# Kernel tuning notes

Measured on AMD Instinct MI355X. Metric: run time of the kernel, lower is better.

Reference implementation:

```python
import jax, jax.numpy as jnp
import numpy as np

GRID = 28
P = GRID * GRID  # 784 grid points
BY = 1.0 / 13.5  # grid spacing from DTMWeightWrapperLayer(by=1/13.5)
_c = BY * np.stack(np.meshgrid(np.arange(GRID), np.arange(GRID), indexing='ij'), -1).reshape(P, 2).astype(np.float32)
_D2np = ((_c[:, None, :] - _c[None, :, :]) ** 2).sum(-1)
_ORDERnp = np.argsort(_D2np, axis=1)  # per-grid-point neighbor order (constant)
D2S = jnp.asarray(np.take_along_axis(_D2np, _ORDERnp, axis=1), dtype=jnp.float32)  # [P,P] sorted sq dists
ORDER = jnp.asarray(_ORDERnp, dtype=jnp.int32)
TSEQ_A = jnp.asarray(np.linspace(0.06, 0.3, 25), dtype=jnp.float32); KK_A = (0, 1)
TSEQ_B = jnp.asarray(np.linspace(0.14, 0.4, 27), dtype=jnp.float32); KK_B = (0, 1, 2)

def _conv(x, k):
    return jax.lax.conv_general_dilated(x, k, (1, 1), 'SAME', dimension_numbers=('NHWC', 'HWIO', 'NHWC'))

def _dtm(w, m0):
    # distance-to-measure: w [B,P] nonneg weights on the 28x28 grid -> dtm values [B,P]
    ws = w[:, ORDER]                      # [B,P,P] weights ordered by distance from each grid point
    cum = jnp.cumsum(ws, axis=-1)
    m0W = m0 * jnp.sum(w, axis=-1)[:, None, None]  # mass threshold per sample
    eff = jnp.clip(m0W - (cum - ws), 0.0, ws)      # effective weight used from each neighbor
    return jnp.sqrt(jnp.sum(eff * D2S[None], axis=-1) / m0W[:, :, 0])

def _topo(f, tseq, kk, W, b):
    # persistence-landscape features: lambda_k(t) = k-th largest tent value over grid points
    tmax = tseq[-1]
    tent = jnp.maximum(0.0, jnp.minimum(tseq[None, :, None] - f[:, None, :], (tmax - tseq)[None, :, None]))  # [B,T,P]
    top, _ = jax.lax.top_k(tent, max(kk) + 1)       # [B,T,kmax]
    lam = top[..., jnp.asarray(kk)]                 # [B,T,|KK|]
    return lam.reshape(f.shape[0], -1) @ W + b

def setup_inputs() -> dict:
    key = jax.random.key(0)
    ks = jax.random.split(key, 16)
    r = lambda i, s: (0.05 * jax.random.normal(ks[i], s)).astype(jnp.float32)
    z = lambda n: jnp.zeros((n,), jnp.float32)
    return {
        'x': jax.random.uniform(ks[0], (16, 28, 28, 1), jnp.float32),
        'k11': r(1, (3, 3, 1, 32)), 'cb11': z(32), 'k12': r(2, (3, 3, 32, 1)), 'cb12': z(1),
        'k31': r(3, (3, 3, 1, 32)), 'cb31': z(32), 'k32': r(4, (3, 3, 32, 1)), 'cb32': z(1),
        'k41': r(5, (3, 3, 1, 32)), 'cb41': z(32), 'k42': r(6, (3, 3, 32, 1)), 'cb42': z(1),
        'W33': r(7, (50, 16)), 'b33': z(16), 'W43': r(8, (81, 16)), 'b43': z(16),
        'W5': r(9, (50, 16)), 'b5': z(16), 'W6': r(10, (81, 16)), 'b6': z(16),
        'W7': r(11, (848, 64)), 'b7': z(64), 'W8': r(12, (64, 10)), 'b8': z(10),
    }

def reference(x, k11, cb11, k12, cb12, k31, cb31, k32, cb32, k41, cb41, k42, cb42,
              W33, b33, W43, b43, W5, b5, W6, b6, W7, b7, W8, b8):
    relu = jax.nn.relu
    B = 16
    # CNN branch on raw image
    x1 = relu(_conv(relu(_conv(x, k11) + cb11), k12) + cb12).reshape(B, P)
    # DTM functions on the grid
    x2 = x.reshape(B, P)
    x2_1 = _dtm(x2, 0.05)
    x2_2 = _dtm(x2, 0.2)
    # CNN on DTM(m0=0.05) then topo layer
    x3 = relu(_conv(relu(_conv(x2_1.reshape(B, GRID, GRID, 1), k31) + cb31), k32) + cb32).reshape(B, P)
    x3 = relu(_topo(x3, TSEQ_A, KK_A, W33, b33))
    # CNN on DTM(m0=0.2) then topo layer
    x4 = relu(_conv(relu(_conv(x2_2.reshape(B, GRID, GRID, 1), k41) + cb41), k42) + cb42).reshape(B, P)
    x4 = relu(_topo(x4, TSEQ_B, KK_B, W43, b43))
    # topo layers directly on DTM functions
    x5 = relu(_topo(x2_1, TSEQ_A, KK_A, W5, b5))
    x6 = relu(_topo(x2_2, TSEQ_B, KK_B, W6, b6))
    xc = jnp.concatenate((x1, x3, x4, x5, x6), axis=-1)  # [16,848]
    return relu(xc @ W7 + b7) @ W8 + b8  # [16,10]
```

## Files before the change

### kernel.cpp

```cpp
#include <hip/hip_runtime.h>
#include <math.h>

#define GRID 28
#define NP 784

struct PairTab { unsigned int pk[NP]; float d2[NP]; };
constexpr PairTab make_pairs() {
    PairTab t{};
    int cnt[1459] = {};
    for (int di = 0; di < GRID; ++di)
        for (int dj = 0; dj < GRID; ++dj) cnt[di*di + dj*dj]++;
    int off[1459] = {};
    int acc = 0;
    for (int s = 0; s < 1459; ++s) { off[s] = acc; acc += cnt[s]; }
    const double BY2 = (1.0/13.5) * (1.0/13.5);
    for (int di = 0; di < GRID; ++di)
        for (int dj = 0; dj < GRID; ++dj) {
            int s = di*di + dj*dj;
            int o = off[s]++;
            t.pk[o] = (unsigned)((di << 8) | dj);
            t.d2[o] = (float)((double)s * BY2);
        }
    return t;
}
__constant__ PairTab d_PT = make_pairs();

__device__ void conv_band(const float* __restrict__ in,
                          const float* __restrict__ kA, const float* __restrict__ cbA,
                          const float* __restrict__ kB, const float* __restrict__ cbB,
                          float* __restrict__ outImg, int r0, float* smem)
{
    float* inl = smem;
    float* kAl = inl + 224;
    float* kBl = kAl + 288;
    float* cbl = kBl + 288;
    float* h   = cbl + 32;
    const int tid = threadIdx.x;
    const float cbB0 = cbB[0];

    if (tid < 288) { kAl[tid] = kA[tid]; kBl[tid] = kB[tid]; }
    else if (tid < 320) cbl[tid - 288] = cbA[tid - 288];
    else if (tid < 320 + 8*GRID) {
        const int i = tid - 320;
        const int lr = i / GRID, xx = i % GRID;
        const int y = r0 - 2 + lr;
        inl[i] = ((unsigned)y < GRID) ? in[y*GRID + xx] : 0.f;
    }
    __syncthreads();

    for (int o = tid; o < 6*GRID*32; o += 1024) {
        const int c = o & 31;
        const int pos = o >> 5;
        const int xx = pos % GRID;
        const int lr = pos / GRID;
        const int y = r0 - 1 + lr;
        if ((unsigned)y < GRID) {
            float a = cbl[c];
            #pragma unroll
            for (int dy = 0; dy < 3; ++dy) {
                const int iy = y + dy - 1;
                if ((unsigned)iy >= GRID) continue;
                const int il = iy - (r0 - 2);
                #pragma unroll
                for (int dx = 0; dx < 3; ++dx) {
                    const int ix = xx + dx - 1;
                    if ((unsigned)ix < GRID)
                        a = fmaf(inl[il*GRID + ix], kAl[(dy*3 + dx)*32 + c], a);
                }
            }
            h[(lr*GRID + xx)*33 + c] = fmaxf(a, 0.f);
        }
    }
    __syncthreads();

    if (tid < 4*4*GRID) {
        const int o = tid >> 2, part = tid & 3;
        const int xx = o % GRID, ly = o / GRID;
        const int y = r0 + ly;
        float a = 0.f;
        #pragma unroll
        for (int dy = 0; dy < 3; ++dy) {
            const int yy = y + dy - 1;
            if ((unsigned)yy >= GRID) continue;
            const int lr = yy - (r0 - 1);
            #pragma unroll
            for (int dx = 0; dx < 3; ++dx) {
                const int x2 = xx + dx - 1;
                if ((unsigned)x2 >= GRID) continue;
                const float* hb = &h[(lr*GRID + x2)*33 + part*8];
                const float* kb = &kBl[(dy*3 + dx)*32 + part*8];
                #pragma unroll
                for (int c = 0; c < 8; ++c) a += hb[c] * kb[c];
            }
        }
        a += __shfl_xor(a, 1, 64);
        a += __shfl_xor(a, 2, 64);
        if (part == 0) outImg[y*GRID + xx] = fmaxf(a + cbB0, 0.f);
    }
}

__global__ __launch_bounds__(1024) void k1_kernel(const float* __restrict__ x,
        const float* __restrict__ k11, const float* __restrict__ cb11,
        const float* __restrict__ k12, const float* __restrict__ cb12,
        float* __restrict__ ws)
{
    __shared__ float smem[6376];
    const int blk = blockIdx.x;
    const int tid = threadIdx.x;

    if (blk < 112) {
        const int img = blk / 7, band = blk % 7;
        conv_band(x + img*NP, k11, cb11, k12, cb12, ws + 25088 + img*NP, band*4, smem);
        return;
    }

    float* wimg = smem;
    float* red  = smem + 784;
    float* out1 = ws;
    float* out2 = ws + 12544;
    const int dblk = blk - 112;
    const int img = dblk / 49, grp = dblk % 49;
    const int w = tid >> 6, lane = tid & 63;

    float v = 0.f;
    if (tid < NP) { v = x[img*NP + tid]; wimg[tid] = v; }
    for (int off = 32; off; off >>= 1) v += __shfl_down(v, off, 64);
    if (lane == 0) red[w] = v;
    __syncthreads();
    float sumw = 0.f;
    #pragma unroll
    for (int i = 0; i < 16; ++i) sumw += red[i];

    const int pix = grp*16 + w;
    const int pr = pix / GRID, pc = pix % GRID;
    const float m0W1 = 0.05f * sumw;
    const float m0W2 = 0.2f  * sumw;
    float a1 = 0.f, a2 = 0.f, carry = 0.f;

    for (int k0 = 0; k0 < NP; k0 += 64) {
        const int idx = k0 + lane;
        const int ii  = idx < NP ? idx : NP-1;
        const unsigned p = d_PT.pk[ii];
        const float dd   = d_PT.d2[ii];
        const int di = (int)(p >> 8);
        const int dj = (int)(p & 255u);
        const int dG = di * GRID;
        const bool rpOK = (pr + di) < GRID;
        const bool rmOK = pr >= di;
        const bool cpOK = (pc + dj) < GRID;
        const bool cmOK = pc >= dj;
        float Wg = 0.f;
        if (rpOK && cpOK)               Wg += wimg[pix + dG + dj];
        if (dj && rpOK && cmOK)         Wg += wimg[pix + dG - dj];
        if (di && rmOK && cpOK)         Wg += wimg[pix - dG + dj];
        if (di && dj && rmOK && cmOK)   Wg += wimg[pix - dG - dj];
        if (idx >= NP) Wg = 0.f;
        float incl = Wg;
        #pragma unroll
        for (int d = 1; d < 64; d <<= 1) {
            const float t = __shfl_up(incl, d, 64);
            if (lane >= d) incl += t;
        }
        const float cumb = carry + (incl - Wg);
        const float e1 = fminf(fmaxf(m0W1 - cumb, 0.f), Wg);
        const float e2 = fminf(fmaxf(m0W2 - cumb, 0.f), Wg);
        a1 = fmaf(e1, dd, a1);
        a2 = fmaf(e2, dd, a2);
        carry += __shfl(incl, 63, 64);
        if (carry >= m0W2) break;
    }
    for (int m = 32; m; m >>= 1) { a1 += __shfl_xor(a1, m, 64); a2 += __shfl_xor(a2, m, 64); }
    if (lane == 0) {
        out1[img*NP + pix] = sqrtf(a1 / m0W1);
        out2[img*NP + pix] = sqrtf(a2 / m0W2);
    }
}

__global__ __launch_bounds__(1024) void k2_kernel(
        const float* __restrict__ k31, const float* __restrict__ cb31,
        const float* __restrict__ k32, const float* __restrict__ cb32,
        const float* __restrict__ k41, const float* __restrict__ cb41,
        const float* __restrict__ k42, const float* __restrict__ cb42,
        float* __restrict__ ws)
{
    __shared__ float smem[6376];
    const int blk = blockIdx.x;
    const float* x2_1 = ws;
    const float* x2_2 = ws + 12544;
    float* x3c = ws + 37632;
    float* x4c = ws + 50176;

    if (blk < 112) {
        const int img = blk / 7, band = blk % 7;
        conv_band(x2_1 + img*NP, k31, cb31, k32, cb32, x3c + img*NP, band*4, smem);
    } else {
        const int c = blk - 112;
        const int img = c / 7, band = c % 7;
        conv_band(x2_2 + img*NP, k41, cb41, k42, cb42, x4c + img*NP, band*4, smem);
    }
}

__device__ __forceinline__ float tseqA(int i) {
    if (i == 24) return 0.3f;
    return (float)((double)i * ((0.3 - 0.06)/24.0) + 0.06);
}
__device__ __forceinline__ float tseqB(int i) {
    if (i == 26) return 0.4f;
    return (float)((double)i * ((0.4 - 0.14)/26.0) + 0.14);
}

__device__ __forceinline__ void merge3(float& m0, float& m1, float& m2,
                                       float b0, float b1, float b2) {
    float r0, r1, r2;
    if (m0 <= b0) {
        r0 = m0;
        if (m1 <= b0) { r1 = m1; r2 = fminf(m2, b0); }
        else          { r1 = b0; r2 = fminf(m1, b1); }
    } else {
        r0 = b0;
        if (b1 <= m0) { r1 = b1; r2 = fminf(b2, m0); }
        else          { r1 = m0; r2 = fminf(m1, b1); }
    }
    m0 = r0; m1 = r1; m2 = r2;
}

__global__ __launch_bounds__(1024) void tail_kernel(
        const float* __restrict__ W33, const float* __restrict__ b33,
        const float* __restrict__ W43, const float* __restrict__ b43,
        const float* __restrict__ W5,  const float* __restrict__ b5,
        const float* __restrict__ W6,  const float* __restrict__ b6,
        const float* __restrict__ W7,  const float* __restrict__ b7,
        const float* __restrict__ W8,  const float* __restrict__ b8,
        const float* __restrict__ ws,  float* __restrict__ out)
{
    __shared__ float xc[848];
    __shared__ float part[1024];
    __shared__ float h7[64];
    __shared__ float fsh[16];
    const int b = blockIdx.x, tid = threadIdx.x;
    const int w = tid >> 6, lane = tid & 63;
    const float* x2_1 = ws;
    const float* x2_2 = ws + 12544;
    const float* x1o  = ws + 25088;
    const float* x3c  = ws + 37632;
    const float* x4c  = ws + 50176;

    if (tid < NP) xc[tid] = x1o[b*NP + tid];

    if (w < 4) {
        const float* src = (w == 0) ? x3c : (w == 1) ? x4c : (w == 2) ? x2_1 : x2_2;
        src += b*NP;
        float m0 = INFINITY, m1 = INFINITY, m2 = INFINITY;
        for (int i = lane; i < NP; i += 64) {
            const float v = src[i];
            if (v < m0)      { m2 = m1; m1 = m0; m0 = v; }
            else if (v < m1) { m2 = m1; m1 = v; }
            else if (v < m2) { m2 = v; }
        }
        for (int mask = 1; mask <= 32; mask <<= 1) {
            const float b0 = __shfl_xor(m0, mask, 64);
            const float b1 = __shfl_xor(m1, mask, 64);
            const float b2 = __shfl_xor(m2, mask, 64);
            merge3(m0, m1, m2, b0, b1, b2);
        }
        if (lane == 0) { fsh[w*3+0] = m0; fsh[w*3+1] = m1; fsh[w*3+2] = m2; }
    }
    __syncthreads();

    if (w < 4) {
        const int g = lane >> 4, j = lane & 15;
        const float f0 = fsh[w*3+0], f1 = fsh[w*3+1], f2 = fsh[w*3+2];
        float acc = 0.f;
        if (w == 0 || w == 2) {
            const float* Wm = (w == 0) ? W33 : W5;
            for (int i = g; i < 50; i += 4) {
                const int t = i >> 1, k = i & 1;
                const float ts = tseqA(t);
                const float fk = k ? f1 : f0;
                const float lam = fmaxf(fminf(ts - fk, 0.3f - ts), 0.f);
                acc = fmaf(lam, Wm[i*16 + j], acc);
            }
        } else {
            const float* Wm = (w == 1) ? W43 : W6;
            for (int i = g; i < 81; i += 4) {
                const int t = i / 3, k = i - t*3;
                const float ts = tseqB(t);
                const float fk = (k == 0) ? f0 : (k == 1 ? f1 : f2);
                const float lam = fmaxf(fminf(ts - fk, 0.4f - ts), 0.f);
                acc = fmaf(lam, Wm[i*16 + j], acc);
            }
        }
        acc += __shfl_xor(acc, 16, 64);
        acc += __shfl_xor(acc, 32, 64);
        if (lane < 16) {
            const float* bv = (w == 0) ? b33 : (w == 1) ? b43 : (w == 2) ? b5 : b6;
            xc[784 + w*16 + lane] = fmaxf(acc + bv[lane], 0.f);
        }
    }
    __syncthreads();

    {
        float acc = 0.f;
        const int i0 = w * 53;
        for (int i = i0; i < i0 + 53; ++i) acc = fmaf(xc[i], W7[i*64 + lane], acc);
        part[w*64 + lane] = acc;
    }
    __syncthreads();
    if (tid < 64) {
        float s = b7[tid];
        #pragma unroll
        for (int k = 0; k < 16; ++k) s += part[k*64 + tid];
        h7[tid] = fmaxf(s, 0.f);
    }
    __syncthreads();

    if (w < 10) {
        float a2 = h7[lane] * W8[lane*10 + w];
        for (int m = 32; m; m >>= 1) a2 += __shfl_down(a2, m, 64);
        if (lane == 0) out[b*10 + w] = a2 + b8[w];
    }
}

extern "C" void kernel_launch(void* const* d_in, const int* in_sizes, int n_in,
                              void* d_out, int out_size, void* d_ws, size_t ws_size,
                              hipStream_t stream)
{
    const float* x    = (const float*)d_in[0];
    const float* k11  = (const float*)d_in[1];
    const float* cb11 = (const float*)d_in[2];
    const float* k12  = (const float*)d_in[3];
    const float* cb12 = (const float*)d_in[4];
    const float* k31  = (const float*)d_in[5];
    const float* cb31 = (const float*)d_in[6];
    const float* k32  = (const float*)d_in[7];
    const float* cb32 = (const float*)d_in[8];
    const float* k41  = (const float*)d_in[9];
    const float* cb41 = (const float*)d_in[10];
    const float* k42  = (const float*)d_in[11];
    const float* cb42 = (const float*)d_in[12];
    const float* W33  = (const float*)d_in[13];
    const float* b33  = (const float*)d_in[14];
    const float* W43  = (const float*)d_in[15];
    const float* b43  = (const float*)d_in[16];
    const float* W5   = (const float*)d_in[17];
    const float* b5   = (const float*)d_in[18];
    const float* W6   = (const float*)d_in[19];
    const float* b6   = (const float*)d_in[20];
    const float* W7   = (const float*)d_in[21];
    const float* b7   = (const float*)d_in[22];
    const float* W8   = (const float*)d_in[23];
    const float* b8   = (const float*)d_in[24];
    float* ws  = (float*)d_ws;
    float* out = (float*)d_out;

    k1_kernel  <<<dim3(896), dim3(1024), 0, stream>>>(x, k11, cb11, k12, cb12, ws);
    k2_kernel  <<<dim3(224), dim3(1024), 0, stream>>>(k31, cb31, k32, cb32,
                                                      k41, cb41, k42, cb42, ws);
    tail_kernel<<<dim3(16),  dim3(1024), 0, stream>>>(W33, b33, W43, b43, W5, b5, W6, b6,
                                                      W7, b7, W8, b8, ws, out);
}
```

Baseline: 32.62 us.

## Rework conv band with padded tiles, register sliding window and float4 loads

The conv band now keeps its input and hidden tiles zero-padded, so the boundary checks in the inner loops go away. Each thread holds the nine first-layer weights and a 3x3 input window in registers and slides the window down six rows, instead of reloading everything from shared memory for each output. The second layer reads the padded hidden tile, which has a stride of 36, with float4 loads, and the launch bounds add a min-blocks hint. The cost is more shared memory and a zero-fill pass over the hidden buffer.

New measurement: 31.36 us. 3.9% less time.

```diff
diff --git a/kernel.cpp b/kernel.cpp
--- a/kernel.cpp
+++ b/kernel.cpp
@@ -25,72 +25,75 @@
 }
 __constant__ PairTab d_PT = make_pairs();
 
+#define CB_SMEM 7328
 __device__ void conv_band(const float* __restrict__ in,
                           const float* __restrict__ kA, const float* __restrict__ cbA,
                           const float* __restrict__ kB, const float* __restrict__ cbB,
                           float* __restrict__ outImg, int r0, float* smem)
 {
     float* inl = smem;
-    float* kAl = inl + 224;
+    float* kAl = inl + 240;
     float* kBl = kAl + 288;
     float* cbl = kBl + 288;
     float* h   = cbl + 32;
     const int tid = threadIdx.x;
     const float cbB0 = cbB[0];
 
-    if (tid < 288) { kAl[tid] = kA[tid]; kBl[tid] = kB[tid]; }
+    if (tid < 288)      { kAl[tid] = kA[tid]; kBl[tid] = kB[tid]; }
     else if (tid < 320) cbl[tid - 288] = cbA[tid - 288];
-    else if (tid < 320 + 8*GRID) {
+    else if (tid < 560) {
         const int i = tid - 320;
-        const int lr = i / GRID, xx = i % GRID;
-        const int y = r0 - 2 + lr;
-        inl[i] = ((unsigned)y < GRID) ? in[y*GRID + xx] : 0.f;
-    }
-    __syncthreads();
-
-    for (int o = tid; o < 6*GRID*32; o += 1024) {
-        const int c = o & 31;
-        const int pos = o >> 5;
-        const int xx = pos % GRID;
-        const int lr = pos / GRID;
-        const int y = r0 - 1 + lr;
-        if ((unsigned)y < GRID) {
-            float a = cbl[c];
-            #pragma unroll
-            for (int dy = 0; dy < 3; ++dy) {
-                const int iy = y + dy - 1;
-                if ((unsigned)iy >= GRID) continue;
-                const int il = iy - (r0 - 2);
-                #pragma unroll
-                for (int dx = 0; dx < 3; ++dx) {
-                    const int ix = xx + dx - 1;
-                    if ((unsigned)ix < GRID)
-                        a = fmaf(inl[il*GRID + ix], kAl[(dy*3 + dx)*32 + c], a);
-                }
+        const int lr = i / 30, col = i % 30;
+        const int y = r0 - 2 + lr, ix = col - 1;
+        inl[i] = ((unsigned)y < GRID && (unsigned)ix < GRID) ? in[y*GRID + ix] : 0.f;
+    }
+    {
+        float4* h4 = (float4*)h;
+        for (int i = tid; i < 6480/4; i += 1024) h4[i] = make_float4(0.f,0.f,0.f,0.f);
+    }
+    __syncthreads();
+
+    if (tid < 896) {
+        const int c = tid & 31, xx = tid >> 5;
+        float ka0 = kAl[0*32+c], ka1 = kAl[1*32+c], ka2 = kAl[2*32+c];
+        float ka3 = kAl[3*32+c], ka4 = kAl[4*32+c], ka5 = kAl[5*32+c];
+        float ka6 = kAl[6*32+c], ka7 = kAl[7*32+c], ka8 = kAl[8*32+c];
+        const float bias = cbl[c];
+        float w00 = inl[0*30+xx], w01 = inl[0*30+xx+1], w02 = inl[0*30+xx+2];
+        float w10 = inl[1*30+xx], w11 = inl[1*30+xx+1], w12 = inl[1*30+xx+2];
+        float w20 = inl[2*30+xx], w21 = inl[2*30+xx+1], w22 = inl[2*30+xx+2];
+        #pragma unroll
+        for (int s = 0; s < 6; ++s) {
+            const int y = r0 - 1 + s;
+            float a = bias;
+            a = fmaf(w00, ka0, a); a = fmaf(w01, ka1, a); a = fmaf(w02, ka2, a);
+            a = fmaf(w10, ka3, a); a = fmaf(w11, ka4, a); a = fmaf(w12, ka5, a);
+            a = fmaf(w20, ka6, a); a = fmaf(w21, ka7, a); a = fmaf(w22, ka8, a);
+            if ((unsigned)y < GRID) h[(s*30 + xx + 1)*36 + c] = fmaxf(a, 0.f);
+            if (s < 5) {
+                w00 = w10; w01 = w11; w02 = w12;
+                w10 = w20; w11 = w21; w12 = w22;
+                w20 = inl[(s+3)*30+xx]; w21 = inl[(s+3)*30+xx+1]; w22 = inl[(s+3)*30+xx+2];
             }
-            h[(lr*GRID + xx)*33 + c] = fmaxf(a, 0.f);
-        }
-    }
-    __syncthreads();
-
-    if (tid < 4*4*GRID) {
-        const int o = tid >> 2, part = tid & 3;
-        const int xx = o % GRID, ly = o / GRID;
+        }
+    }
+    __syncthreads();
+
+    if (tid < 448) {
+        const int part = tid & 3, o = tid >> 2;
+        const int xx = o % 28, ly = o / 28;
         const int y = r0 + ly;
         float a = 0.f;
         #pragma unroll
         for (int dy = 0; dy < 3; ++dy) {
-            const int yy = y + dy - 1;
-            if ((unsigned)yy >= GRID) continue;
-            const int lr = yy - (r0 - 1);
             #pragma unroll
             for (int dx = 0; dx < 3; ++dx) {
-                const int x2 = xx + dx - 1;
-                if ((unsigned)x2 >= GRID) continue;
-                const float* hb = &h[(lr*GRID + x2)*33 + part*8];
-                const float* kb = &kBl[(dy*3 + dx)*32 + part*8];
-                #pragma unroll
-                for (int c = 0; c < 8; ++c) a += hb[c] * kb[c];
+                const float4* hb = (const float4*)&h[((ly+dy)*30 + xx+dx)*36 + part*8];
+                const float4* kb = (const float4*)&kBl[(dy*3+dx)*32 + part*8];
+                const float4 h0 = hb[0], h1 = hb[1];
+                const float4 k0 = kb[0], k1 = kb[1];
+                a += h0.x*k0.x; a += h0.y*k0.y; a += h0.z*k0.z; a += h0.w*k0.w;
+                a += h1.x*k1.x; a += h1.y*k1.y; a += h1.z*k1.z; a += h1.w*k1.w;
             }
         }
         a += __shfl_xor(a, 1, 64);
@@ -99,12 +102,12 @@
     }
 }
 
-__global__ __launch_bounds__(1024) void k1_kernel(const float* __restrict__ x,
+__global__ __launch_bounds__(1024, 8) void k1_kernel(const float* __restrict__ x,
         const float* __restrict__ k11, const float* __restrict__ cb11,
         const float* __restrict__ k12, const float* __restrict__ cb12,
         float* __restrict__ ws)
 {
-    __shared__ float smem[6376];
+    __shared__ float smem[CB_SMEM];
     const int blk = blockIdx.x;
     const int tid = threadIdx.x;
 
@@ -176,14 +179,14 @@
     }
 }
 
-__global__ __launch_bounds__(1024) void k2_kernel(
+__global__ __launch_bounds__(1024, 8) void k2_kernel(
         const float* __restrict__ k31, const float* __restrict__ cb31,
         const float* __restrict__ k32, const float* __restrict__ cb32,
         const float* __restrict__ k41, const float* __restrict__ cb41,
         const float* __restrict__ k42, const float* __restrict__ cb42,
         float* __restrict__ ws)
 {
-    __shared__ float smem[6376];
+    __shared__ float smem[CB_SMEM];
     const int blk = blockIdx.x;
     const float* x2_1 = ws;
     const float* x2_2 = ws + 12544;
```
